# Performance work log

Hardware: AMD Instinct MI355X
Metric: run time of the kernel (lower is better)

## Reference

```python
import jax, jax.numpy as jnp
import numpy as np

C, H, W, D, M = 64, 512, 512, 4, 16


def setup_inputs() -> dict:
    key = jax.random.key(0)
    ks = jax.random.split(key, 9)
    scale = (1.0 / (C * C)) ** 0.5
    return {
        "q": jax.random.normal(ks[0], (1, 1, H, W), jnp.float32),
        "proj_w": jax.random.normal(ks[1], (C, 1, 1, 1), jnp.float32),
        "proj_b": jax.random.normal(ks[2], (C, 1, 1), jnp.float32) * 0.01,
        "spec_wr": jax.random.normal(ks[3], (D, C, C, M, M), jnp.float32) * scale,
        "spec_wi": jax.random.normal(ks[4], (D, C, C, M, M), jnp.float32) * scale,
        "w_w": jax.random.normal(ks[5], (D, C, C, 1, 1), jnp.float32) * (1.0 / C ** 0.5),
        "w_b": jax.random.normal(ks[6], (D, C, 1, 1), jnp.float32) * 0.01,
        "final_w": jax.random.normal(ks[7], (1, C, 1, 1), jnp.float32) * (1.0 / C ** 0.5),
        "final_b": jax.random.normal(ks[8], (1, 1, 1), jnp.float32) * 0.01,
    }


def _spectral(x, wr, wi, m):
    # x: (C,H,W). FFT2 -> contract low modes -> zero-pad -> iFFT2, take real part.
    Cin, Hh, Ww = x.shape
    x_ft = jnp.fft.fft2(x, axes=(-2, -1))  # (C,H,W) complex
    w = (wr + 1j * wi).astype(x_ft.dtype)  # (Cin,Cout,m,m)
    out_sub = jnp.einsum('imn,iomn->omn', x_ft[:, :m, :m], w)
    out_ft = jnp.zeros((wr.shape[1], Hh, Ww), dtype=x_ft.dtype).at[:, :m, :m].set(out_sub)
    return jnp.fft.ifft2(out_ft, axes=(-2, -1)).real


def reference(q, proj_w, proj_b, spec_wr, spec_wi, w_w, w_b, final_w, final_b):
    m = spec_wr.shape[-1]
    depth = spec_wr.shape[0]
    x = q[0].astype(jnp.float32)  # (C_in,H,W) -- batch must be 1
    # 1x1 conv lift
    x = jnp.einsum('oi,ihw->ohw', proj_w[:, :, 0, 0], x) + proj_b
    for d in range(depth):
        x_spec = _spectral(x, spec_wr[d], spec_wi[d], m)
        x_local = jnp.einsum('oi,ihw->ohw', w_w[d, :, :, 0, 0], x) + w_b[d]
        x = jax.nn.gelu(x_spec + x_local)
    x = jnp.einsum('oi,ihw->ohw', final_w[:, :, 0, 0], x) + final_b
    return x[None]  # re-add batch dim
```

## Files before the change

kernel.cpp:

```cpp
#include <hip/hip_runtime.h>
#include <cmath>

#define CC 64
#define HH 512
#define WWID 512
#define HWSZ (HH*WWID)
#define DEPTH 4

typedef __attribute__((ext_vector_type(8))) short short8;
typedef __attribute__((ext_vector_type(4))) float floatx4;

__device__ inline unsigned short f2bf(float f){
  unsigned int u = __float_as_uint(f);
  u += 0x7FFF + ((u >> 16) & 1);
  return (unsigned short)(u >> 16);
}
__device__ inline float bf2f(unsigned short h){
  return __uint_as_float(((unsigned int)h) << 16);
}

__global__ void k_init(const float* __restrict__ ww,
                       float* __restrict__ ctab, float* __restrict__ stab,
                       unsigned short* __restrict__ trigBh, unsigned short* __restrict__ trigBl,
                       unsigned short* __restrict__ trigTh, unsigned short* __restrict__ trigTl,
                       unsigned short* __restrict__ Whi, unsigned short* __restrict__ Wlo,
                       float4* __restrict__ Xfz){
  if (blockIdx.x < 32) Xfz[blockIdx.x*256 + threadIdx.x] = make_float4(0.f,0.f,0.f,0.f);
  int idx = blockIdx.x*256 + threadIdx.x;
  if (idx < 8192){
    int pos = idx >> 4, k = idx & 15;
    int r = (pos * k) & 511;
    double ang = (2.0 * 3.14159265358979323846 / 512.0) * (double)r;
    float c = (float)cos(ang), s = (float)sin(ang);
    ctab[idx] = c;  stab[idx] = s;
    unsigned short ch = f2bf(c), sh = f2bf(s);
    unsigned short cl = f2bf(c - bf2f(ch)), sl = f2bf(s - bf2f(sh));
    trigBh[pos*32 + 2*k]     = ch;  trigBl[pos*32 + 2*k]     = cl;
    trigBh[pos*32 + 2*k + 1] = sh;  trigBl[pos*32 + 2*k + 1] = sl;
    trigTh[(2*k)*512 + pos]   = ch;  trigTl[(2*k)*512 + pos]   = cl;
    trigTh[(2*k+1)*512 + pos] = sh;  trigTl[(2*k+1)*512 + pos] = sl;
  } else {
    int t = idx - 8192;
    float v = ww[t];
    unsigned short h = f2bf(v);
    Whi[t] = h;  Wlo[t] = f2bf(v - bf2f(h));
  }
}

#define XPITCH 33
#define BPITCH 520
template<int LIFT>
__global__ __launch_bounds__(256) void k_dftw(const unsigned int* __restrict__ xp,
    const float* __restrict__ qsrc, const float* __restrict__ pw, const float* __restrict__ pb,
    const unsigned short* __restrict__ trigTh, const unsigned short* __restrict__ trigTl,
    const float* __restrict__ ctab, const float* __restrict__ stab,
    float* __restrict__ Xfa, float4* __restrict__ Yz){
  if (blockIdx.x < 32) Yz[blockIdx.x*256 + threadIdx.x] = make_float4(0.f,0.f,0.f,0.f);

  __shared__ unsigned short Bhs[32*BPITCH], Bls[32*BPITCH];
  __shared__ float X1s[64*XPITCH];
  int row0 = blockIdx.x * 64;
  int i  = row0 >> 9;
  int h0 = row0 & 511;
  int t = threadIdx.x;
  int g = t >> 6, lm = t & 15, lq = (t >> 4) & 3;
  float pa = 0.f, pbv = 0.f;
  if (LIFT){ pa = pw[i]; pbv = pb[i]; }

  {
    #pragma unroll
    for (int u = 0; u < 8; ++u){
      int idx = u*256 + t;
      int row = idx >> 6, ck = (idx & 63)*8;
      *(uint4*)&Bhs[row*BPITCH + ck] = *(const uint4*)(trigTh + row*512 + ck);
      *(uint4*)&Bls[row*BPITCH + ck] = *(const uint4*)(trigTl + row*512 + ck);
    }
  }
  __syncthreads();

  floatx4 acc[2] = {{0.f,0.f,0.f,0.f},{0.f,0.f,0.f,0.f}};

  int hrow = h0 + g*16 + lm;
  const unsigned int* arow = xp + ((size_t)hrow*64 + i)*512;
  const float*        qrow = qsrc + (size_t)hrow*512;

  #pragma unroll 4
  for (int ch = 0; ch < 16; ++ch){
    int kb = ch*32 + lq*8;
    short8 ah, al;
    if (LIFT){
      float4 qa = *(const float4*)(qrow + kb);
      float4 qb = *(const float4*)(qrow + kb + 4);
      float v[8] = {qa.x,qa.y,qa.z,qa.w,qb.x,qb.y,qb.z,qb.w};
      unsigned int hs[4], ls[4];
      #pragma unroll
      for (int p = 0; p < 4; ++p){
        float v0 = fmaf(pa, v[2*p],   pbv);
        float v1 = fmaf(pa, v[2*p+1], pbv);
        unsigned short hh0 = f2bf(v0), hh1 = f2bf(v1);
        unsigned short gg0 = f2bf(v0 - bf2f(hh0)), gg1 = f2bf(v1 - bf2f(hh1));
        hs[p] = (unsigned)hh0 | ((unsigned)hh1 << 16);
        ls[p] = (unsigned)gg0 | ((unsigned)gg1 << 16);
      }
      ah = *(short8*)hs;  al = *(short8*)ls;
    } else {
      uint4 va = *(const uint4*)(arow + kb);
      uint4 vb = *(const uint4*)(arow + kb + 4);
      unsigned int u[8] = {va.x,va.y,va.z,va.w,vb.x,vb.y,vb.z,vb.w};
      unsigned int hs[4], ls[4];
      #pragma unroll
      for (int p = 0; p < 4; ++p){
        hs[p] = (u[2*p] & 0xffffu) | (u[2*p+1] << 16);
        ls[p] = (u[2*p] >> 16)     | (u[2*p+1] & 0xffff0000u);
      }
      ah = *(short8*)hs;  al = *(short8*)ls;
    }
    #pragma unroll
    for (int nt = 0; nt < 2; ++nt){
      int j = nt*16 + lm;
      short8 bh = *(const short8*)&Bhs[j*BPITCH + kb];
      short8 bl = *(const short8*)&Bls[j*BPITCH + kb];
      acc[nt] = __builtin_amdgcn_mfma_f32_16x16x32_bf16(ah, bh, acc[nt], 0, 0, 0);
      acc[nt] = __builtin_amdgcn_mfma_f32_16x16x32_bf16(ah, bl, acc[nt], 0, 0, 0);
      acc[nt] = __builtin_amdgcn_mfma_f32_16x16x32_bf16(al, bh, acc[nt], 0, 0, 0);
    }
  }

  __syncthreads();
  #pragma unroll
  for (int nt = 0; nt < 2; ++nt){
    int j = nt*16 + lm;
    float sgn = (j & 1) ? -1.f : 1.f;
    #pragma unroll
    for (int rg = 0; rg < 4; ++rg){
      int m = g*16 + lq*4 + rg;
      X1s[m*XPITCH + j] = sgn * acc[nt][rg];
    }
  }
  __syncthreads();

  int mo = t >> 4, n = t & 15;
  float ar = 0.f, ai = 0.f;
  #pragma unroll 8
  for (int hh = 0; hh < 64; ++hh){
    int h = h0 + hh;
    float Re = X1s[hh*XPITCH + 2*n];
    float Im = X1s[hh*XPITCH + 2*n + 1];
    float c = ctab[h*16 + mo], s = stab[h*16 + mo];
    ar += Re*c + Im*s;
    ai += Im*c - Re*s;
  }
  atomicAdd(&Xfa[(i*256 + t)*2],     ar);
  atomicAdd(&Xfa[(i*256 + t)*2 + 1], ai);
}

__global__ void k_contract(const float2* __restrict__ Xf,
                           const float* __restrict__ wr, const float* __restrict__ wi,
                           float* __restrict__ Ya){
  int o = blockIdx.x, ic = blockIdx.y;
  int mn = blockIdx.z*64 + threadIdx.x;
  float ar = 0.f, ai = 0.f;
  int i0 = ic * 16;
  #pragma unroll
  for (int ii = 0; ii < 16; ++ii){
    int i = i0 + ii;
    float2 xf = Xf[i*256 + mn];
    float wrv = wr[(i*64 + o)*256 + mn];
    float wiv = wi[(i*64 + o)*256 + mn];
    ar += xf.x*wrv - xf.y*wiv;
    ai += xf.x*wiv + xf.y*wrv;
  }
  const float sc = 1.f/262144.f;
  atomicAdd(&Ya[(o*256 + mn)*2],     ar*sc);
  atomicAdd(&Ya[(o*256 + mn)*2 + 1], ai*sc);
}

__global__ void k_idfth(const float2* __restrict__ Y, const float* __restrict__ ct,
                        const float* __restrict__ st,
                        unsigned int* __restrict__ Thi, unsigned int* __restrict__ Tlo,
                        float4* __restrict__ Xfz){
  if (blockIdx.x < 32) Xfz[blockIdx.x*256 + threadIdx.x] = make_float4(0.f,0.f,0.f,0.f);
  int idx = blockIdx.x*256 + threadIdx.x;
  int n = idx & 15, o = (idx >> 4) & 63, h = idx >> 10;
  float ar = 0.f, ai = 0.f;
  #pragma unroll
  for (int m = 0; m < 16; ++m){
    float2 y = Y[(o<<8) + (m<<4) + n];
    float c = ct[h*16 + m], s = st[h*16 + m];
    ar += y.x*c - y.y*s;
    ai += y.x*s + y.y*c;
  }
  float tr = ar, ts = -ai;
  unsigned short rh = f2bf(tr), sh = f2bf(ts);
  Thi[idx] = (unsigned int)rh | ((unsigned int)sh << 16);
  unsigned short rl = f2bf(tr - bf2f(rh)), slr = f2bf(ts - bf2f(sh));
  Tlo[idx] = (unsigned int)rl | ((unsigned int)slr << 16);
}

#define PITCH 104
template<int LIFT, int FINAL>
__global__ __launch_bounds__(256, 4) void k_combine(
    const unsigned int* __restrict__ xp, const float* __restrict__ qsrc,
    const float* __restrict__ pw, const float* __restrict__ pb,
    const unsigned short* __restrict__ Whid, const unsigned short* __restrict__ Wlod,
    const unsigned int* __restrict__ Thi,  const unsigned int* __restrict__ Tlo,
    const unsigned short* __restrict__ trigBh, const unsigned short* __restrict__ trigBl,
    const float* __restrict__ wb, unsigned int* __restrict__ xo,
    const float* __restrict__ fw, const float* __restrict__ fb,
    float* __restrict__ outp)
{
  __shared__ unsigned short Ah[64*PITCH], Al[64*PITCH];
  int h  = blockIdx.y;
  int w0 = blockIdx.x * 128;
  int t  = threadIdx.x;

  {
    int o = t >> 2, q8 = t & 3;
    const uint4* sh = (const uint4*)((const unsigned int*)Whid + o*32 + q8*8);
    const uint4* sl = (const uint4*)((const unsigned int*)Wlod + o*32 + q8*8);
    uint4* dh = (uint4*)((unsigned int*)&Ah[o*PITCH] + q8*8);
    uint4* dl = (uint4*)((unsigned int*)&Al[o*PITCH] + q8*8);
    dh[0] = sh[0]; dh[1] = sh[1];
    dl[0] = sl[0]; dl[1] = sl[1];
  }
  {
    int o = t >> 2, q4 = t & 3;
    const uint4* sh = (const uint4*)(Thi + (size_t)h*1024 + o*16 + q4*4);
    const uint4* sl = (const uint4*)(Tlo + (size_t)h*1024 + o*16 + q4*4);
    uint4* dh = (uint4*)((unsigned int*)&Ah[o*PITCH + 64] + q4*4);
    uint4* dl = (uint4*)((unsigned int*)&Al[o*PITCH + 64] + q4*4);
    dh[0] = sh[0];
    dl[0] = sl[0];
  }
  __syncthreads();

  int g  = t >> 6;
  int lm = t & 15;
  int lq = (t >> 4) & 3;
  int wbase = w0 + g*32;

  const unsigned int* xw = xp + (size_t)h*32768;
  float pwv[16], pbv[16];
  if (LIFT){
    #pragma unroll
    for (int u = 0; u < 8; ++u){
      pwv[u]   = pw[lq*8 + u];      pbv[u]   = pb[lq*8 + u];
      pwv[8+u] = pw[32 + lq*8 + u]; pbv[8+u] = pb[32 + lq*8 + u];
    }
  }

  floatx4 acc[8] = {{0.f,0.f,0.f,0.f},{0.f,0.f,0.f,0.f},{0.f,0.f,0.f,0.f},{0.f,0.f,0.f,0.f},
                    {0.f,0.f,0.f,0.f},{0.f,0.f,0.f,0.f},{0.f,0.f,0.f,0.f},{0.f,0.f,0.f,0.f}};

  #pragma unroll
  for (int nt = 0; nt < 2; ++nt){
    int w = wbase + nt*16 + lm;
    unsigned int v0[8], v1[8];
    if (LIFT){
      float qv = qsrc[(size_t)h*512 + w];
      #pragma unroll
      for (int u = 0; u < 8; ++u){
        float a = fmaf(pwv[u], qv, pbv[u]);
        unsigned short hh = f2bf(a), ll = f2bf(a - bf2f(hh));
        v0[u] = (unsigned int)hh | ((unsigned int)ll << 16);
        float b = fmaf(pwv[8+u], qv, pbv[8+u]);
        unsigned short hb = f2bf(b), lb = f2bf(b - bf2f(hb));
        v1[u] = (unsigned int)hb | ((unsigned int)lb << 16);
      }
    } else {
      #pragma unroll
      for (int u = 0; u < 8; ++u){
        v0[u] = xw[(size_t)(     lq*8 + u)*512 + w];
        v1[u] = xw[(size_t)(32 + lq*8 + u)*512 + w];
      }
    }
    unsigned int f0[4], l0[4], f1[4], l1[4];
    #pragma unroll
    for (int p = 0; p < 4; ++p){
      f0[p] = (v0[2*p] & 0xffffu) | (v0[2*p+1] << 16);
      l0[p] = (v0[2*p] >> 16)     | (v0[2*p+1] & 0xffff0000u);
      f1[p] = (v1[2*p] & 0xffffu) | (v1[2*p+1] << 16);
      l1[p] = (v1[2*p] >> 16)     | (v1[2*p+1] & 0xffff0000u);
    }
    short8 bf0 = *(short8*)f0, bl0 = *(short8*)l0;
    short8 bf1 = *(short8*)f1, bl1 = *(short8*)l1;
    short8 bf2 = *(const short8*)(trigBh + (size_t)w*32 + lq*8);
    short8 bl2 = *(const short8*)(trigBl + (size_t)w*32 + lq*8);

    #pragma unroll
    for (int m = 0; m < 4; ++m){
      short8 af0 = *(const short8*)&Ah[(m*16 + lm)*PITCH +  0 + lq*8];
      short8 al0 = *(const short8*)&Al[(m*16 + lm)*PITCH +  0 + lq*8];
      short8 af1 = *(const short8*)&Ah[(m*16 + lm)*PITCH + 32 + lq*8];
      short8 al1 = *(const short8*)&Al[(m*16 + lm)*PITCH + 32 + lq*8];
      short8 af2 = *(const short8*)&Ah[(m*16 + lm)*PITCH + 64 + lq*8];
      short8 al2 = *(const short8*)&Al[(m*16 + lm)*PITCH + 64 + lq*8];
      int a = m*2 + nt;
      acc[a] = __builtin_amdgcn_mfma_f32_16x16x32_bf16(af0, bf0, acc[a], 0, 0, 0);
      acc[a] = __builtin_amdgcn_mfma_f32_16x16x32_bf16(af0, bl0, acc[a], 0, 0, 0);
      acc[a] = __builtin_amdgcn_mfma_f32_16x16x32_bf16(al0, bf0, acc[a], 0, 0, 0);
      acc[a] = __builtin_amdgcn_mfma_f32_16x16x32_bf16(af1, bf1, acc[a], 0, 0, 0);
      acc[a] = __builtin_amdgcn_mfma_f32_16x16x32_bf16(af1, bl1, acc[a], 0, 0, 0);
      acc[a] = __builtin_amdgcn_mfma_f32_16x16x32_bf16(al1, bf1, acc[a], 0, 0, 0);
      acc[a] = __builtin_amdgcn_mfma_f32_16x16x32_bf16(af2, bf2, acc[a], 0, 0, 0);
      acc[a] = __builtin_amdgcn_mfma_f32_16x16x32_bf16(af2, bl2, acc[a], 0, 0, 0);
      acc[a] = __builtin_amdgcn_mfma_f32_16x16x32_bf16(al2, bf2, acc[a], 0, 0, 0);
    }
  }

  if (!FINAL){
    #pragma unroll
    for (int m = 0; m < 4; ++m){
      #pragma unroll
      for (int nt = 0; nt < 2; ++nt){
        int w = wbase + nt*16 + lm;
        #pragma unroll
        for (int rg = 0; rg < 4; ++rg){
          int o = m*16 + lq*4 + rg;
          float u = acc[m*2+nt][rg] + wb[o];
          float z = 0.7978845608028654f * fmaf(0.044715f, u*u*u, u);
          float e = __expf(2.f*z);
          float gl = u - __fdividef(u, e + 1.f);
          unsigned short hi_ = f2bf(gl);
          unsigned short lo_ = f2bf(gl - bf2f(hi_));
          xo[((size_t)h*64 + o)*512 + w] = (unsigned int)hi_ | ((unsigned int)lo_ << 16);
        }
      }
    }
  } else {
    float* fred = (float*)Ah;
    __syncthreads();
    #pragma unroll
    for (int nt = 0; nt < 2; ++nt){
      float partial = 0.f;
      #pragma unroll
      for (int m = 0; m < 4; ++m){
        #pragma unroll
        for (int rg = 0; rg < 4; ++rg){
          int o = m*16 + lq*4 + rg;
          float u = acc[m*2+nt][rg] + wb[o];
          float z = 0.7978845608028654f * fmaf(0.044715f, u*u*u, u);
          float e = __expf(2.f*z);
          float gl = u - __fdividef(u, e + 1.f);
          partial = fmaf(fw[o], gl, partial);
        }
      }
      int wl = g*32 + nt*16 + lm;
      fred[wl*17 + lq] = partial;
    }
    __syncthreads();
    if (t < 128){
      float s = fb[0];
      #pragma unroll
      for (int k2 = 0; k2 < 4; ++k2) s += fred[t*17 + k2];
      outp[(size_t)h*512 + w0 + t] = s;
    }
  }
}

extern "C" void kernel_launch(void* const* d_in, const int* in_sizes, int n_in,
                              void* d_out, int out_size, void* d_ws, size_t ws_size,
                              hipStream_t stream) {
  const float* q       = (const float*)d_in[0];
  const float* proj_w  = (const float*)d_in[1];
  const float* proj_b  = (const float*)d_in[2];
  const float* spec_wr = (const float*)d_in[3];
  const float* spec_wi = (const float*)d_in[4];
  const float* w_w     = (const float*)d_in[5];
  const float* w_b     = (const float*)d_in[6];
  const float* final_w = (const float*)d_in[7];
  const float* final_b = (const float*)d_in[8];
  float* out = (float*)d_out;

  char* ws = (char*)d_ws;
  float*  ctab = (float*) (ws + 0);
  float*  stab = (float*) (ws + 32768);
  unsigned short* trigBh = (unsigned short*)(ws + 65536);
  unsigned short* trigBl = (unsigned short*)(ws + 98304);
  unsigned int* Thi = (unsigned int*)(ws + 131072);
  unsigned int* Tlo = (unsigned int*)(ws + 2228224);
  float*  Xf   = (float*) (ws + 4325376);
  float*  Y    = (float*) (ws + 4456448);
  unsigned int* x = (unsigned int*)(ws + 4587520);
  unsigned short* Whi = (unsigned short*)(ws + 71696384);
  unsigned short* Wlo = (unsigned short*)(ws + 71729152);
  unsigned short* trigTh = (unsigned short*)(ws + 71761920);
  unsigned short* trigTl = (unsigned short*)(ws + 71794688);

  k_init<<<96, 256, 0, stream>>>(w_w, ctab, stab, trigBh, trigBl, trigTh, trigTl,
                                 Whi, Wlo, (float4*)Xf);

  for (int d = 0; d < DEPTH; ++d){
    if (d == 0)
      k_dftw<1><<<512, 256, 0, stream>>>(x, q, proj_w, proj_b, trigTh, trigTl,
                                         ctab, stab, Xf, (float4*)Y);
    else
      k_dftw<0><<<512, 256, 0, stream>>>(x, q, proj_w, proj_b, trigTh, trigTl,
                                         ctab, stab, Xf, (float4*)Y);
    k_contract<<<dim3(64,4,4), 64, 0, stream>>>((const float2*)Xf,
                                                spec_wr + (size_t)d*1048576,
                                                spec_wi + (size_t)d*1048576, Y);
    k_idfth<<<2048, 256, 0, stream>>>((const float2*)Y, ctab, stab, Thi, Tlo,
                                      (float4*)Xf);
    if (d == 0)
      k_combine<1,0><<<dim3(4,512), 256, 0, stream>>>(x, q, proj_w, proj_b,
          Whi + d*4096, Wlo + d*4096, Thi, Tlo, trigBh, trigBl,
          w_b + d*64, x, final_w, final_b, out);
    else if (d < DEPTH-1)
      k_combine<0,0><<<dim3(4,512), 256, 0, stream>>>(x, q, proj_w, proj_b,
          Whi + d*4096, Wlo + d*4096, Thi, Tlo, trigBh, trigBl,
          w_b + d*64, x, final_w, final_b, out);
    else
      k_combine<0,1><<<dim3(4,512), 256, 0, stream>>>(x, q, proj_w, proj_b,
          Whi + d*4096, Wlo + d*4096, Thi, Tlo, trigBh, trigBl,
          w_b + d*64, x, final_w, final_b, out);
  }
}
```

Before: 318.4 us.

## Fuse spectral contraction with inverse H-DFT into one kernel per layer

Merges the mode contraction and the inverse row-DFT into a single kernel with one block per output channel. The contracted modes are kept in shared memory, which removes the atomic accumulation into Y, its zero-fill, and one kernel launch per layer. Zeroing of the Xf accumulator moves into the combine kernel. In exchange the new kernel runs only 64 blocks with long serial loops, which cuts parallelism for this stage.

```diff
diff --git a/kernel.cpp b/kernel.cpp
--- a/kernel.cpp
+++ b/kernel.cpp
@@ -54,9 +54,7 @@
     const float* __restrict__ qsrc, const float* __restrict__ pw, const float* __restrict__ pb,
     const unsigned short* __restrict__ trigTh, const unsigned short* __restrict__ trigTl,
     const float* __restrict__ ctab, const float* __restrict__ stab,
-    float* __restrict__ Xfa, float4* __restrict__ Yz){
-  if (blockIdx.x < 32) Yz[blockIdx.x*256 + threadIdx.x] = make_float4(0.f,0.f,0.f,0.f);
-
+    float* __restrict__ Xfa){
   __shared__ unsigned short Bhs[32*BPITCH], Bls[32*BPITCH];
   __shared__ float X1s[64*XPITCH];
   int row0 = blockIdx.x * 64;
@@ -154,47 +152,45 @@
   atomicAdd(&Xfa[(i*256 + t)*2 + 1], ai);
 }
 
-__global__ void k_contract(const float2* __restrict__ Xf,
-                           const float* __restrict__ wr, const float* __restrict__ wi,
-                           float* __restrict__ Ya){
-  int o = blockIdx.x, ic = blockIdx.y;
-  int mn = blockIdx.z*64 + threadIdx.x;
+__global__ __launch_bounds__(256) void k_spec(const float2* __restrict__ Xf,
+    const float* __restrict__ wr, const float* __restrict__ wi,
+    const float* __restrict__ ct, const float* __restrict__ st,
+    unsigned int* __restrict__ Thi, unsigned int* __restrict__ Tlo){
+  __shared__ float2 Ys[256];
+  int o = blockIdx.x, t = threadIdx.x;
   float ar = 0.f, ai = 0.f;
-  int i0 = ic * 16;
-  #pragma unroll
-  for (int ii = 0; ii < 16; ++ii){
-    int i = i0 + ii;
-    float2 xf = Xf[i*256 + mn];
-    float wrv = wr[(i*64 + o)*256 + mn];
-    float wiv = wi[(i*64 + o)*256 + mn];
+  const float* wrb = wr + (size_t)o*256 + t;
+  const float* wib = wi + (size_t)o*256 + t;
+  #pragma unroll 8
+  for (int i = 0; i < 64; ++i){
+    float2 xf = Xf[i*256 + t];
+    float wrv = wrb[(size_t)i*16384];
+    float wiv = wib[(size_t)i*16384];
     ar += xf.x*wrv - xf.y*wiv;
     ai += xf.x*wiv + xf.y*wrv;
   }
   const float sc = 1.f/262144.f;
-  atomicAdd(&Ya[(o*256 + mn)*2],     ar*sc);
-  atomicAdd(&Ya[(o*256 + mn)*2 + 1], ai*sc);
-}
-
-__global__ void k_idfth(const float2* __restrict__ Y, const float* __restrict__ ct,
-                        const float* __restrict__ st,
-                        unsigned int* __restrict__ Thi, unsigned int* __restrict__ Tlo,
-                        float4* __restrict__ Xfz){
-  if (blockIdx.x < 32) Xfz[blockIdx.x*256 + threadIdx.x] = make_float4(0.f,0.f,0.f,0.f);
-  int idx = blockIdx.x*256 + threadIdx.x;
-  int n = idx & 15, o = (idx >> 4) & 63, h = idx >> 10;
-  float ar = 0.f, ai = 0.f;
-  #pragma unroll
-  for (int m = 0; m < 16; ++m){
-    float2 y = Y[(o<<8) + (m<<4) + n];
-    float c = ct[h*16 + m], s = st[h*16 + m];
-    ar += y.x*c - y.y*s;
-    ai += y.x*s + y.y*c;
-  }
-  float tr = ar, ts = -ai;
-  unsigned short rh = f2bf(tr), sh = f2bf(ts);
-  Thi[idx] = (unsigned int)rh | ((unsigned int)sh << 16);
-  unsigned short rl = f2bf(tr - bf2f(rh)), slr = f2bf(ts - bf2f(sh));
-  Tlo[idx] = (unsigned int)rl | ((unsigned int)slr << 16);
+  Ys[t] = make_float2(ar*sc, ai*sc);
+  __syncthreads();
+
+  int n = t & 15, hs = t >> 4;
+  for (int hh = 0; hh < 32; ++hh){
+    int h = hs*32 + hh;
+    float tr_ = 0.f, ti_ = 0.f;
+    #pragma unroll
+    for (int m = 0; m < 16; ++m){
+      float2 y = Ys[(m<<4) + n];
+      float c = ct[h*16 + m], s = st[h*16 + m];
+      tr_ += y.x*c - y.y*s;
+      ti_ += y.x*s + y.y*c;
+    }
+    float tr = tr_, ts = -ti_;
+    unsigned short rh = f2bf(tr), sh2 = f2bf(ts);
+    int idx = (h*64 + o)*16 + n;
+    Thi[idx] = (unsigned int)rh | ((unsigned int)sh2 << 16);
+    unsigned short rl = f2bf(tr - bf2f(rh)), slr = f2bf(ts - bf2f(sh2));
+    Tlo[idx] = (unsigned int)rl | ((unsigned int)slr << 16);
+  }
 }
 
 #define PITCH 104
@@ -207,12 +203,15 @@
     const unsigned short* __restrict__ trigBh, const unsigned short* __restrict__ trigBl,
     const float* __restrict__ wb, unsigned int* __restrict__ xo,
     const float* __restrict__ fw, const float* __restrict__ fb,
-    float* __restrict__ outp)
+    float* __restrict__ outp, float4* __restrict__ Xfz)
 {
   __shared__ unsigned short Ah[64*PITCH], Al[64*PITCH];
   int h  = blockIdx.y;
   int w0 = blockIdx.x * 128;
   int t  = threadIdx.x;
+
+  if (!FINAL && blockIdx.x == 0 && h < 32)
+    Xfz[h*256 + t] = make_float4(0.f,0.f,0.f,0.f);
 
   {
     int o = t >> 2, q8 = t & 3;
@@ -380,7 +379,6 @@
   unsigned int* Thi = (unsigned int*)(ws + 131072);
   unsigned int* Tlo = (unsigned int*)(ws + 2228224);
   float*  Xf   = (float*) (ws + 4325376);
-  float*  Y    = (float*) (ws + 4456448);
   unsigned int* x = (unsigned int*)(ws + 4587520);
   unsigned short* Whi = (unsigned short*)(ws + 71696384);
   unsigned short* Wlo = (unsigned short*)(ws + 71729152);
@@ -393,26 +391,25 @@
   for (int d = 0; d < DEPTH; ++d){
     if (d == 0)
       k_dftw<1><<<512, 256, 0, stream>>>(x, q, proj_w, proj_b, trigTh, trigTl,
-                                         ctab, stab, Xf, (float4*)Y);
+                                         ctab, stab, Xf);
     else
       k_dftw<0><<<512, 256, 0, stream>>>(x, q, proj_w, proj_b, trigTh, trigTl,
-                                         ctab, stab, Xf, (float4*)Y);
-    k_contract<<<dim3(64,4,4), 64, 0, stream>>>((const float2*)Xf,
-                                                spec_wr + (size_t)d*1048576,
-                                                spec_wi + (size_t)d*1048576, Y);
-    k_idfth<<<2048, 256, 0, stream>>>((const float2*)Y, ctab, stab, Thi, Tlo,
-                                      (float4*)Xf);
+                                         ctab, stab, Xf);
+    k_spec<<<64, 256, 0, stream>>>((const float2*)Xf,
+                                   spec_wr + (size_t)d*1048576,
+                                   spec_wi + (size_t)d*1048576,
+                                   ctab, stab, Thi, Tlo);
     if (d == 0)
       k_combine<1,0><<<dim3(4,512), 256, 0, stream>>>(x, q, proj_w, proj_b,
           Whi + d*4096, Wlo + d*4096, Thi, Tlo, trigBh, trigBl,
-          w_b + d*64, x, final_w, final_b, out);
+          w_b + d*64, x, final_w, final_b, out, (float4*)Xf);
     else if (d < DEPTH-1)
       k_combine<0,0><<<dim3(4,512), 256, 0, stream>>>(x, q, proj_w, proj_b,
           Whi + d*4096, Wlo + d*4096, Thi, Tlo, trigBh, trigBl,
-          w_b + d*64, x, final_w, final_b, out);
+          w_b + d*64, x, final_w, final_b, out, (float4*)Xf);
     else
       k_combine<0,1><<<dim3(4,512), 256, 0, stream>>>(x, q, proj_w, proj_b,
           Whi + d*4096, Wlo + d*4096, Thi, Tlo, trigBh, trigBl,
-          w_b + d*64, x, final_w, final_b, out);
-  }
-}
+          w_b + d*64, x, final_w, final_b, out, (float4*)Xf);
+  }
+}
```

Result: slower. 409.6 us (+28.6%).
